# Kernel optimization log

Hardware: AMD Instinct MI355X
Metric: run time of the kernel (lower is better)

The kernel has to match this reference:

```python
import jax, jax.numpy as jnp
import numpy as np

N_NODES = 100000
N_EDGES = 1600000
D_IN = 128
D_OUT = 128
N_GRAPHS = 256


def setup_inputs() -> dict:
    key = jax.random.key(0)
    k1, k2, k3, k4 = jax.random.split(key, 4)
    H = jax.random.normal(k1, (N_NODES, D_IN), dtype=jnp.float32)
    edge_index = jax.random.randint(k2, (2, N_EDGES), 0, N_NODES, dtype=jnp.int64)
    batch = jnp.sort(jax.random.randint(k3, (N_NODES,), 0, N_GRAPHS, dtype=jnp.int64))
    # Kaiming-normal init: std = sqrt(2 / fan_in)
    W = jax.random.normal(k4, (D_IN, D_OUT), dtype=jnp.float32) * np.float32(np.sqrt(2.0 / D_IN))
    return {"H": H, "edge_index": edge_index, "batch": batch, "W": W}


def reference(H, edge_index, batch, W):
    N = H.shape[0]
    src, dst = edge_index[0], edge_index[1]
    # message passing: gather source features, scatter_add into destinations
    agg = jax.ops.segment_sum(H[src], dst, num_segments=N)  # [N, D]
    out = H + agg
    # virtual node: per-graph mean, broadcast back to nodes
    sums = jax.ops.segment_sum(out, batch, num_segments=N_GRAPHS)            # [G, D]
    counts = jax.ops.segment_sum(jnp.ones((N, 1), out.dtype), batch,
                                 num_segments=N_GRAPHS)                       # [G, 1]
    vmean = sums / jnp.maximum(counts, 1.0)
    out = out + vmean[batch]
    # dense transform + activation
    return jax.nn.relu(out @ W)
```

## Files before the change

### kernel.cpp

```cpp
#include <hip/hip_runtime.h>

#define DIM 128
#define NGRAPH 256

#define CHUNK 512
#define CHB 9
#define MAXNB 256
#define EPB 4096
#define EPT (EPB / 256)
#define FCAP 14336

typedef __attribute__((ext_vector_type(8))) short short8;
typedef __attribute__((ext_vector_type(4))) float f32x4;

__device__ inline unsigned int bpack2(float lo, float hi) {
  unsigned int ul = __float_as_uint(lo);
  unsigned int uh = __float_as_uint(hi);
  ul = (ul + 0x7fffu + ((ul >> 16) & 1u)) >> 16;
  uh = (uh + 0x7fffu + ((uh >> 16) & 1u)) & 0xffff0000u;
  return ul | uh;
}

__device__ inline float4 bunpack4(uint2 v) {
  float4 r;
  r.x = __uint_as_float(v.x << 16);
  r.y = __uint_as_float(v.x & 0xffff0000u);
  r.z = __uint_as_float(v.y << 16);
  r.w = __uint_as_float(v.y & 0xffff0000u);
  return r;
}

__global__ __launch_bounds__(256) void k_prep(const float4* __restrict__ H4,
    uint2* __restrict__ Hb, int n4,
    const int* __restrict__ dst, unsigned short* __restrict__ bh, int E,
    int NBLK) {
  __shared__ unsigned int hist[MAXNB];
  int blk = blockIdx.x, t = threadIdx.x;
  int i = blk * 256 + t;
  if (i < n4) {
    float4 a = H4[i];
    uint2 r;
    r.x = bpack2(a.x, a.y);
    r.y = bpack2(a.z, a.w);
    Hb[i] = r;
  }
  if (blk < NBLK) {
    hist[t] = 0;
    __syncthreads();
    int base = blk * EPB;
#pragma unroll
    for (int k = 0; k < EPT; ++k) {
      int e = base + k * 256 + t;
      if (e < E) atomicAdd(&hist[((unsigned)dst[e]) >> CHB], 1);
    }
    __syncthreads();
    bh[(size_t)blk * MAXNB + t] = (unsigned short)hist[t];
  }
}

__global__ __launch_bounds__(256) void k_bhist(const int* __restrict__ dst,
    unsigned short* __restrict__ bh, int E) {
  __shared__ unsigned int hist[MAXNB];
  int blk = blockIdx.x, t = threadIdx.x;
  hist[t] = 0;
  __syncthreads();
  int base = blk * EPB;
#pragma unroll
  for (int i = 0; i < EPT; ++i) {
    int e = base + i * 256 + t;
    if (e < E) atomicAdd(&hist[((unsigned)dst[e]) >> CHB], 1);
  }
  __syncthreads();
  bh[(size_t)blk * MAXNB + t] = (unsigned short)hist[t];
}

__global__ __launch_bounds__(256) void k_bscan(unsigned short* __restrict__ bh,
    unsigned int* __restrict__ btot, int NBLK) {
  __shared__ unsigned int tmp[256];
  int b = blockIdx.x, t = threadIdx.x;
  int i0 = 2 * t, i1 = 2 * t + 1;
  unsigned int a0 = (i0 < NBLK) ? bh[(size_t)i0 * MAXNB + b] : 0u;
  unsigned int a1 = (i1 < NBLK) ? bh[(size_t)i1 * MAXNB + b] : 0u;
  unsigned int ps = a0 + a1;
  tmp[t] = ps;
  __syncthreads();
  for (int off = 1; off < 256; off <<= 1) {
    unsigned int x = (t >= off) ? tmp[t - off] : 0u;
    __syncthreads();
    tmp[t] += x;
    __syncthreads();
  }
  unsigned int ex = tmp[t] - ps;
  if (i0 < NBLK) bh[(size_t)i0 * MAXNB + b] = (unsigned short)ex;
  if (i1 < NBLK) bh[(size_t)i1 * MAXNB + b] = (unsigned short)(ex + a0);
  if (t == 255) btot[b] = tmp[255];
}

__global__ __launch_bounds__(256) void k_bscan2(const unsigned int* __restrict__ btot,
    unsigned int* __restrict__ bbase, int* __restrict__ offs, int N, int E) {
  __shared__ unsigned int s[256];
  int t = threadIdx.x;
  unsigned int v = btot[t];
  s[t] = v;
  __syncthreads();
  for (int off = 1; off < 256; off <<= 1) {
    unsigned int x = (t >= off) ? s[t - off] : 0u;
    __syncthreads();
    s[t] += x;
    __syncthreads();
  }
  bbase[t] = s[t] - v;
  if (t == 255) { bbase[256] = s[255]; offs[N] = E; }
}

__global__ __launch_bounds__(256) void k_part(const int* __restrict__ src,
    const int* __restrict__ dst, const unsigned short* __restrict__ bh,
    const unsigned int* __restrict__ bbase, unsigned int* __restrict__ pack, int E) {
  __shared__ unsigned int hist[MAXNB];
  __shared__ unsigned int sc[MAXNB];
  __shared__ unsigned int gbase[MAXNB];
  __shared__ unsigned int lpack[EPB];
  __shared__ unsigned short lbkt[EPB];
  __shared__ unsigned int totS;
  int blk = blockIdx.x, t = threadIdx.x;
  hist[t] = 0;
  __syncthreads();

  int base = blk * EPB;
  unsigned int pk[EPT];
  int bk[EPT];
  unsigned int rk[EPT];
#pragma unroll
  for (int i = 0; i < EPT; ++i) {
    int e = base + i * 256 + t;
    if (e < E) {
      unsigned int s = (unsigned)src[e], d = (unsigned)dst[e];
      pk[i] = (s << CHB) | (d & (CHUNK - 1));
      int b = (int)(d >> CHB);
      bk[i] = b;
      rk[i] = atomicAdd(&hist[b], 1u);
    } else {
      bk[i] = -1;
    }
  }
  __syncthreads();

  unsigned int c = hist[t];
  sc[t] = c;
  __syncthreads();
  for (int off = 1; off < 256; off <<= 1) {
    unsigned int x = (t >= off) ? sc[t - off] : 0u;
    __syncthreads();
    sc[t] += x;
    __syncthreads();
  }
  if (t == 255) totS = sc[255];
  hist[t] = sc[t] - c;
  gbase[t] = bbase[t] + (unsigned int)bh[(size_t)blk * MAXNB + t];
  __syncthreads();

#pragma unroll
  for (int i = 0; i < EPT; ++i) {
    if (bk[i] >= 0) {
      unsigned int slot = hist[bk[i]] + rk[i];
      lpack[slot] = pk[i];
      lbkt[slot] = (unsigned short)bk[i];
    }
  }
  __syncthreads();

  unsigned int tot = totS;
  for (unsigned int s = t; s < tot; s += 256) {
    int b = lbkt[s];
    unsigned int local = s - hist[b];
    pack[gbase[b] + local] = lpack[s];
  }
}

__global__ __launch_bounds__(256) void k_fine(unsigned int* __restrict__ pack,
    const unsigned int* __restrict__ bbase, int* __restrict__ offs, int N) {
  __shared__ unsigned int lp[FCAP];
  __shared__ unsigned int cnt[CHUNK];
  __shared__ unsigned int cur[CHUNK];
  __shared__ unsigned int tmp[256];
  int b = blockIdx.x, t = threadIdx.x;
  unsigned int lo = bbase[b], hi = bbase[b + 1];
  int n = (int)(hi - lo);
  if (n > FCAP) n = FCAP;
  cnt[2 * t] = 0; cnt[2 * t + 1] = 0;
  __syncthreads();
  for (int i = t; i < n; i += 256) {
    unsigned int p = pack[lo + i];
    lp[i] = p;
    atomicAdd(&cnt[p & (CHUNK - 1)], 1u);
  }
  __syncthreads();
  unsigned int c0 = cnt[2 * t], c1 = cnt[2 * t + 1];
  unsigned int ps = c0 + c1;
  tmp[t] = ps;
  __syncthreads();
  for (int off = 1; off < 256; off <<= 1) {
    unsigned int x = (t >= off) ? tmp[t - off] : 0u;
    __syncthreads();
    tmp[t] += x;
    __syncthreads();
  }
  unsigned int ex = tmp[t] - ps;
  cur[2 * t] = ex;
  cur[2 * t + 1] = ex + c0;
  __syncthreads();
  int nb0 = b * CHUNK;
#pragma unroll
  for (int j = t; j < CHUNK; j += 256) {
    int node = nb0 + j;
    if (node < N) offs[node] = (int)(lo + cur[j]);
  }
  __syncthreads();
  for (int i = t; i < n; i += 256) {
    unsigned int p = lp[i];
    unsigned int r = atomicAdd(&cur[p & (CHUNK - 1)], 1u);
    pack[lo + r] = p;
  }
}

__device__ inline void bacc(uint2 v, float4& a) {
  a.x += __uint_as_float(v.x << 16);
  a.y += __uint_as_float(v.x & 0xffff0000u);
  a.z += __uint_as_float(v.y << 16);
  a.w += __uint_as_float(v.y & 0xffff0000u);
}

__global__ __launch_bounds__(256) void k_gatherbx(const uint2* __restrict__ Hb,
    const int* __restrict__ offs, const unsigned int* __restrict__ pack,
    uint2* __restrict__ Hx, int n) {
  int gid = blockIdx.x * 256 + threadIdx.x;
  int node = gid >> 6;
  if (node >= n) return;
  int lane = threadIdx.x & 63;
  int half = lane >> 5, q = lane & 31;
  float4 A = {0,0,0,0}, B = {0,0,0,0}, C = {0,0,0,0}, D = {0,0,0,0};
  int beg = offs[node], end = offs[node + 1];
  int j = beg + half;
  for (; j + 6 < end; j += 8) {
    uint2 v0 = Hb[(size_t)(pack[j + 0] >> CHB) * 32 + q];
    uint2 v1 = Hb[(size_t)(pack[j + 2] >> CHB) * 32 + q];
    uint2 v2 = Hb[(size_t)(pack[j + 4] >> CHB) * 32 + q];
    uint2 v3 = Hb[(size_t)(pack[j + 6] >> CHB) * 32 + q];
    bacc(v0, A); bacc(v1, B); bacc(v2, C); bacc(v3, D);
  }
  for (; j < end; j += 2) bacc(Hb[(size_t)(pack[j] >> CHB) * 32 + q], A);
  A.x += B.x + (C.x + D.x);
  A.y += B.y + (C.y + D.y);
  A.z += B.z + (C.z + D.z);
  A.w += B.w + (C.w + D.w);
  A.x += __shfl_xor(A.x, 32);
  A.y += __shfl_xor(A.y, 32);
  A.z += __shfl_xor(A.z, 32);
  A.w += __shfl_xor(A.w, 32);
  if (half == 0) {
    float4 b4 = bunpack4(Hb[(size_t)node * 32 + q]);
    uint2 o;
    o.x = bpack2(b4.x + A.x, b4.y + A.y);
    o.y = bpack2(b4.z + A.z, b4.w + A.w);
    Hx[(size_t)node * 32 + q] = o;
  }
}

__global__ __launch_bounds__(256) void k_gatherb(const float* __restrict__ H,
    const uint2* __restrict__ Hb, const int* __restrict__ offs,
    const unsigned int* __restrict__ pack, float* __restrict__ out, int n) {
  int gid = blockIdx.x * 256 + threadIdx.x;
  int node = gid >> 6;
  if (node >= n) return;
  int lane = threadIdx.x & 63;
  int half = lane >> 5, q = lane & 31;
  float4 A = {0,0,0,0}, B = {0,0,0,0}, C = {0,0,0,0}, D = {0,0,0,0};
  int beg = offs[node], end = offs[node + 1];
  int j = beg + half;
  for (; j + 6 < end; j += 8) {
    uint2 v0 = Hb[(size_t)(pack[j + 0] >> CHB) * 32 + q];
    uint2 v1 = Hb[(size_t)(pack[j + 2] >> CHB) * 32 + q];
    uint2 v2 = Hb[(size_t)(pack[j + 4] >> CHB) * 32 + q];
    uint2 v3 = Hb[(size_t)(pack[j + 6] >> CHB) * 32 + q];
    bacc(v0, A); bacc(v1, B); bacc(v2, C); bacc(v3, D);
  }
  for (; j < end; j += 2) bacc(Hb[(size_t)(pack[j] >> CHB) * 32 + q], A);
  A.x += B.x + (C.x + D.x);
  A.y += B.y + (C.y + D.y);
  A.z += B.z + (C.z + D.z);
  A.w += B.w + (C.w + D.w);
  A.x += __shfl_xor(A.x, 32);
  A.y += __shfl_xor(A.y, 32);
  A.z += __shfl_xor(A.z, 32);
  A.w += __shfl_xor(A.w, 32);
  if (half == 0) {
    float4 b4 = ((const float4*)H)[(size_t)node * 32 + q];
    float4 r;
    r.x = b4.x + A.x; r.y = b4.y + A.y; r.z = b4.z + A.z; r.w = b4.w + A.w;
    ((float4*)out)[(size_t)node * 32 + q] = r;
  }
}

__global__ __launch_bounds__(256) void k_gather(const float* __restrict__ H,
    const int* __restrict__ offs, const unsigned int* __restrict__ pack,
    float* __restrict__ out, int n) {
  int gid = blockIdx.x * 256 + threadIdx.x;
  int node = gid >> 6;
  if (node >= n) return;
  int lane = threadIdx.x & 63;
  const float2* H2 = (const float2*)H;
  float2 base = H2[(size_t)node * 64 + lane];
  float2 s0 = {0.f, 0.f}, s1 = {0.f, 0.f};
  int beg = offs[node], end = offs[node + 1];
  int j = beg;
  for (; j + 2 <= end; j += 2) {
    float2 v0 = H2[(size_t)(pack[j + 0] >> CHB) * 64 + lane];
    float2 v1 = H2[(size_t)(pack[j + 1] >> CHB) * 64 + lane];
    s0.x += v0.x; s0.y += v0.y;
    s1.x += v1.x; s1.y += v1.y;
  }
  for (; j < end; ++j) {
    float2 v = H2[(size_t)(pack[j] >> CHB) * 64 + lane];
    s0.x += v.x; s0.y += v.y;
  }
  float2 r;
  r.x = base.x + s0.x + s1.x;
  r.y = base.y + s0.y + s1.y;
  ((float2*)out)[(size_t)node * 64 + lane] = r;
}

__global__ __launch_bounds__(256) void k_init(const float4* __restrict__ s,
                                              float4* __restrict__ d, int n4) {
  int i = blockIdx.x * 256 + threadIdx.x;
  if (i < n4) d[i] = s[i];
}

__global__ __launch_bounds__(256) void k_scatter(const float* __restrict__ H,
    const int* __restrict__ src, const int* __restrict__ dst,
    float* __restrict__ out, int nE) {
  long long idx = (long long)blockIdx.x * 256 + threadIdx.x;
  int e = (int)(idx >> 5);
  if (e >= nE) return;
  int q = (int)(idx & 31);
  int s = src[e];
  int t = dst[e];
  const float4 h = *(const float4*)(H + (size_t)s * DIM + q * 4);
  float* o = out + (size_t)t * DIM + q * 4;
  unsafeAtomicAdd(o + 0, h.x);
  unsafeAtomicAdd(o + 1, h.y);
  unsafeAtomicAdd(o + 2, h.z);
  unsafeAtomicAdd(o + 3, h.w);
}

__global__ __launch_bounds__(256) void k_vmean4x(const uint2* __restrict__ hx,
    const int* __restrict__ batch, float* __restrict__ vmean, int n) {
  int g = blockIdx.x >> 2, c = blockIdx.x & 3;
  int lo = 0, hi = n;
  while (lo < hi) { int m = (lo + hi) >> 1; if (batch[m] < g) lo = m + 1; else hi = m; }
  int start = lo;
  hi = n;
  while (lo < hi) { int m = (lo + hi) >> 1; if (batch[m] < g + 1) lo = m + 1; else hi = m; }
  int end = lo;

  int t = threadIdx.x, rg = t >> 3, s = t & 7;
  int d4 = c * 8 + s;
  float4 acc = {0,0,0,0};
  for (int r = start + rg; r < end; r += 32) {
    float4 v = bunpack4(hx[(size_t)r * 32 + d4]);
    acc.x += v.x; acc.y += v.y; acc.z += v.z; acc.w += v.w;
  }
  __shared__ float4 sd[256];
  sd[t] = acc;
  __syncthreads();
  for (int off = 16; off >= 1; off >>= 1) {
    if (rg < off) {
      float4 o = sd[t + off * 8];
      acc.x += o.x; acc.y += o.y; acc.z += o.z; acc.w += o.w;
      sd[t] = acc;
    }
    __syncthreads();
  }
  if (rg == 0) {
    float cnt = fmaxf((float)(end - start), 1.0f);
    float4 r;
    r.x = acc.x / cnt; r.y = acc.y / cnt; r.z = acc.z / cnt; r.w = acc.w / cnt;
    ((float4*)vmean)[g * 32 + d4] = r;
  }
}

__global__ __launch_bounds__(256) void k_vmean4(const float* __restrict__ x,
    const int* __restrict__ batch, float* __restrict__ vmean, int n) {
  int g = blockIdx.x >> 2, c = blockIdx.x & 3;
  int lo = 0, hi = n;
  while (lo < hi) { int m = (lo + hi) >> 1; if (batch[m] < g) lo = m + 1; else hi = m; }
  int start = lo;
  hi = n;
  while (lo < hi) { int m = (lo + hi) >> 1; if (batch[m] < g + 1) lo = m + 1; else hi = m; }
  int end = lo;

  int t = threadIdx.x, rg = t >> 3, s = t & 7;
  int d4 = c * 8 + s;
  const float4* x4 = (const float4*)x;
  float4 acc = {0,0,0,0};
  for (int r = start + rg; r < end; r += 32) {
    float4 v = x4[(size_t)r * 32 + d4];
    acc.x += v.x; acc.y += v.y; acc.z += v.z; acc.w += v.w;
  }
  __shared__ float4 sd[256];
  sd[t] = acc;
  __syncthreads();
  for (int off = 16; off >= 1; off >>= 1) {
    if (rg < off) {
      float4 o = sd[t + off * 8];
      acc.x += o.x; acc.y += o.y; acc.z += o.z; acc.w += o.w;
      sd[t] = acc;
    }
    __syncthreads();
  }
  if (rg == 0) {
    float cnt = fmaxf((float)(end - start), 1.0f);
    float4 r;
    r.x = acc.x / cnt; r.y = acc.y / cnt; r.z = acc.z / cnt; r.w = acc.w / cnt;
    ((float4*)vmean)[g * 32 + d4] = r;
  }
}

__global__ __launch_bounds__(256) void k_wprep(const float* __restrict__ W,
                                               uint4* __restrict__ wt) {
  int gid = blockIdx.x * 256 + threadIdx.x;
  int col = gid >> 4, chunk = gid & 15;
  float f[8];
#pragma unroll
  for (int j = 0; j < 8; ++j) f[j] = W[(chunk * 8 + j) * DIM + col];
  uint4 u;
  u.x = bpack2(f[0], f[1]);
  u.y = bpack2(f[2], f[3]);
  u.z = bpack2(f[4], f[5]);
  u.w = bpack2(f[6], f[7]);
  wt[col * 16 + (chunk ^ (col & 7))] = u;
}

__global__ __launch_bounds__(256) void k_mfmax(const uint4* __restrict__ Hx,
    float* __restrict__ io, const int* __restrict__ batch,
    const float* __restrict__ vmean, const uint4* __restrict__ wt, int n) {
  __shared__ uint4 WtL[2048];
  int tid = threadIdx.x;
#pragma unroll
  for (int j = 0; j < 8; ++j) WtL[tid + 256 * j] = wt[tid + 256 * j];
  __syncthreads();

  int wid = tid >> 6;
  int lane = tid & 63;
  int q = lane & 15, hi = lane >> 4;
  int row0 = blockIdx.x * 128 + wid * 32;

  f32x4 acc[2][8];
#pragma unroll
  for (int m = 0; m < 2; ++m)
#pragma unroll
    for (int nn = 0; nn < 8; ++nn) acc[m][nn] = (f32x4){0.f, 0.f, 0.f, 0.f};

  bool okm[2];
  const uint4* xrow[2];
  const float4* vrow[2];
#pragma unroll
  for (int m = 0; m < 2; ++m) {
    int row = row0 + m * 16 + q;
    bool ok = row < n;
    okm[m] = ok;
    int g = ok ? batch[row] : 0;
    xrow[m] = Hx + (size_t)row * 16;
    vrow[m] = (const float4*)vmean + (size_t)g * 32;
  }

  for (int kk = 0; kk < 4; ++kk) {
    short8 Bf[8];
#pragma unroll
    for (int nn = 0; nn < 8; ++nn) {
      int colrow = nn * 16 + q;
      int idx = colrow * 16 + ((kk * 4 + hi) ^ (colrow & 7));
      Bf[nn] = *(short8*)&WtL[idx];
    }
    short8 Af[2];
#pragma unroll
    for (int m = 0; m < 2; ++m) {
      uint4 u = {0, 0, 0, 0};
      if (okm[m]) {
        uint4 xv = xrow[m][kk * 4 + hi];
        float4 x0 = bunpack4(*(uint2*)&xv.x);
        float4 x1 = bunpack4(*(uint2*)&xv.z);
        int c = kk * 8 + hi * 2;
        float4 v0 = vrow[m][c], v1 = vrow[m][c + 1];
        u.x = bpack2(x0.x + v0.x, x0.y + v0.y);
        u.y = bpack2(x0.z + v0.z, x0.w + v0.w);
        u.z = bpack2(x1.x + v1.x, x1.y + v1.y);
        u.w = bpack2(x1.z + v1.z, x1.w + v1.w);
      }
      Af[m] = *(short8*)&u;
    }
#pragma unroll
    for (int nn = 0; nn < 8; ++nn) {
      acc[0][nn] = __builtin_amdgcn_mfma_f32_16x16x32_bf16(Af[0], Bf[nn], acc[0][nn], 0, 0, 0);
      acc[1][nn] = __builtin_amdgcn_mfma_f32_16x16x32_bf16(Af[1], Bf[nn], acc[1][nn], 0, 0, 0);
    }
  }

#pragma unroll
  for (int m = 0; m < 2; ++m) {
    int grow0 = row0 + m * 16 + hi * 4;
#pragma unroll
    for (int nn = 0; nn < 8; ++nn) {
      int gcol = nn * 16 + q;
      f32x4 c = acc[m][nn];
#pragma unroll
      for (int r = 0; r < 4; ++r) {
        int grow = grow0 + r;
        if (grow < n) io[(size_t)grow * DIM + gcol] = fmaxf(c[r], 0.f);
      }
    }
  }
}

__global__ __launch_bounds__(256) void k_mfma(float* __restrict__ io,
    const int* __restrict__ batch, const float* __restrict__ vmean,
    const uint4* __restrict__ wt, int n) {
  __shared__ uint4 WtL[2048];
  int tid = threadIdx.x;
#pragma unroll
  for (int j = 0; j < 8; ++j) WtL[tid + 256 * j] = wt[tid + 256 * j];
  __syncthreads();

  int wid = tid >> 6;
  int lane = tid & 63;
  int q = lane & 15, hi = lane >> 4;
  int row0 = blockIdx.x * 128 + wid * 32;

  f32x4 acc[2][8];
#pragma unroll
  for (int m = 0; m < 2; ++m)
#pragma unroll
    for (int nn = 0; nn < 8; ++nn) acc[m][nn] = (f32x4){0.f, 0.f, 0.f, 0.f};

  bool okm[2];
  const float4* xrow[2];
  const float4* vrow[2];
#pragma unroll
  for (int m = 0; m < 2; ++m) {
    int row = row0 + m * 16 + q;
    bool ok = row < n;
    okm[m] = ok;
    int g = ok ? batch[row] : 0;
    xrow[m] = (const float4*)io + (size_t)row * 32;
    vrow[m] = (const float4*)vmean + (size_t)g * 32;
  }

  for (int kk = 0; kk < 4; ++kk) {
    short8 Bf[8];
#pragma unroll
    for (int nn = 0; nn < 8; ++nn) {
      int colrow = nn * 16 + q;
      int idx = colrow * 16 + ((kk * 4 + hi) ^ (colrow & 7));
      Bf[nn] = *(short8*)&WtL[idx];
    }
    short8 Af[2];
#pragma unroll
    for (int m = 0; m < 2; ++m) {
      float4 x0 = {0,0,0,0}, x1 = {0,0,0,0};
      if (okm[m]) {
        int c = kk * 8 + hi * 2;
        float4 a0 = xrow[m][c], a1 = xrow[m][c + 1];
        float4 v0 = vrow[m][c], v1 = vrow[m][c + 1];
        x0.x = a0.x + v0.x; x0.y = a0.y + v0.y; x0.z = a0.z + v0.z; x0.w = a0.w + v0.w;
        x1.x = a1.x + v1.x; x1.y = a1.y + v1.y; x1.z = a1.z + v1.z; x1.w = a1.w + v1.w;
      }
      uint4 u;
      u.x = bpack2(x0.x, x0.y);
      u.y = bpack2(x0.z, x0.w);
      u.z = bpack2(x1.x, x1.y);
      u.w = bpack2(x1.z, x1.w);
      Af[m] = *(short8*)&u;
    }
#pragma unroll
    for (int nn = 0; nn < 8; ++nn) {
      acc[0][nn] = __builtin_amdgcn_mfma_f32_16x16x32_bf16(Af[0], Bf[nn], acc[0][nn], 0, 0, 0);
      acc[1][nn] = __builtin_amdgcn_mfma_f32_16x16x32_bf16(Af[1], Bf[nn], acc[1][nn], 0, 0, 0);
    }
  }

#pragma unroll
  for (int m = 0; m < 2; ++m) {
    int grow0 = row0 + m * 16 + hi * 4;
#pragma unroll
    for (int nn = 0; nn < 8; ++nn) {
      int gcol = nn * 16 + q;
      f32x4 c = acc[m][nn];
#pragma unroll
      for (int r = 0; r < 4; ++r) {
        int grow = grow0 + r;
        if (grow < n) io[(size_t)grow * DIM + gcol] = fmaxf(c[r], 0.f);
      }
    }
  }
}

#define TRR 64
__global__ __launch_bounds__(256) void k_gemm(float* __restrict__ io,
    const int* __restrict__ batch, const float* __restrict__ vmean,
    const float* __restrict__ W, int n) {
  __shared__ float xs[TRR][DIM + 1];
  __shared__ float Wl[DIM][64];
  int tid = threadIdx.x;
  int row0 = blockIdx.x * TRR;

  for (int i = tid; i < TRR * 32; i += 256) {
    int r = i >> 5, c4 = i & 31;
    int row = row0 + r;
    float4 a;
    if (row < n) {
      int g = batch[row];
      float4 xv = *((const float4*)(io + (size_t)row * DIM) + c4);
      float4 vv = *((const float4*)(vmean + (size_t)g * DIM) + c4);
      a.x = xv.x + vv.x; a.y = xv.y + vv.y; a.z = xv.z + vv.z; a.w = xv.w + vv.w;
    } else {
      a.x = a.y = a.z = a.w = 0.f;
    }
    xs[r][c4 * 4 + 0] = a.x;
    xs[r][c4 * 4 + 1] = a.y;
    xs[r][c4 * 4 + 2] = a.z;
    xs[r][c4 * 4 + 3] = a.w;
  }

  int cg = tid & 15;
  int rg = tid >> 4;
  float acc[4][4];

  for (int jh = 0; jh < 2; ++jh) {
    __syncthreads();
    for (int i = tid; i < DIM * 16; i += 256) {
      int k = i >> 4, c4 = i & 15;
      *(float4*)&Wl[k][c4 * 4] =
          *(const float4*)(W + (size_t)k * DIM + jh * 64 + c4 * 4);
    }
    __syncthreads();

#pragma unroll
    for (int a = 0; a < 4; ++a)
#pragma unroll
      for (int b = 0; b < 4; ++b) acc[a][b] = 0.f;

    for (int k = 0; k < DIM; ++k) {
      float4 wv = *(const float4*)&Wl[k][cg * 4];
#pragma unroll
      for (int a = 0; a < 4; ++a) {
        float xv = xs[rg * 4 + a][k];
        acc[a][0] += xv * wv.x;
        acc[a][1] += xv * wv.y;
        acc[a][2] += xv * wv.z;
        acc[a][3] += xv * wv.w;
      }
    }

#pragma unroll
    for (int a = 0; a < 4; ++a) {
      int row = row0 + rg * 4 + a;
      if (row < n) {
        float4 o;
        o.x = fmaxf(acc[a][0], 0.f);
        o.y = fmaxf(acc[a][1], 0.f);
        o.z = fmaxf(acc[a][2], 0.f);
        o.w = fmaxf(acc[a][3], 0.f);
        *(float4*)(io + (size_t)row * DIM + jh * 64 + cg * 4) = o;
      }
    }
  }
}

extern "C" void kernel_launch(void* const* d_in, const int* in_sizes, int n_in,
                              void* d_out, int out_size, void* d_ws, size_t ws_size,
                              hipStream_t stream) {
  const float* H     = (const float*)d_in[0];
  const int*   ei    = (const int*)d_in[1];
  const int*   batch = (const int*)d_in[2];
  const float* W     = (const float*)d_in[3];
  float* out = (float*)d_out;

  int N = in_sizes[0] / DIM;
  int E = in_sizes[1] / 2;
  const int* src = ei;
  const int* dst = ei + E;

  int NB   = (N + CHUNK - 1) >> CHB;
  int NBLK = (E + EPB - 1) / EPB;

  size_t o = 0;
  auto carve = [&](size_t bytes) -> void* {
    void* p = (char*)d_ws + o;
    o = (o + bytes + 255) & ~(size_t)255;
    return p;
  };
  unsigned int*   pack  = (unsigned int*)carve((size_t)E * 4);
  int*            offs  = (int*)carve(((size_t)N + 1) * 4);
  unsigned short* bh    = (unsigned short*)carve((size_t)NBLK * MAXNB * 2);
  unsigned int*   btot  = (unsigned int*)carve(MAXNB * 4);
  unsigned int*   bbase = (unsigned int*)carve((MAXNB + 1) * 4);
  size_t o_csr = o;
  uint2*          Hb    = (uint2*)carve((size_t)N * DIM * 2);
  size_t o_bf = o;
  uint4*          wt    = (uint4*)carve((size_t)DIM * DIM * 2);
  size_t o_wt = o;
  uint2*          Hx    = (uint2*)carve((size_t)N * DIM * 2);
  size_t o_hx = o;
  float* vmean = (float*)bh;

  bool csr_ok = (o_csr <= ws_size) && (NB >= 1) && (NB <= MAXNB) &&
                (NBLK <= 512) && ((size_t)NBLK * MAXNB * 2 >= (size_t)NGRAPH * DIM * 4) &&
                (E / NB <= 8192);
  bool bf_ok = csr_ok && (o_bf <= ws_size);
  bool wt_ok = bf_ok && (o_wt <= ws_size) && (DIM == 128);
  bool hx_ok = wt_ok && (o_hx <= ws_size);

  if (csr_ok) {
    if (bf_ok) {
      int n4 = N * DIM / 4;
      int gprep = (n4 + 255) / 256;
      if (gprep < NBLK) gprep = NBLK;
      k_prep<<<gprep, 256, 0, stream>>>((const float4*)H, Hb, n4, dst, bh, E, NBLK);
    } else {
      k_bhist<<<NBLK, 256, 0, stream>>>(dst, bh, E);
    }
    k_bscan<<<MAXNB, 256, 0, stream>>>(bh, btot, NBLK);
    k_bscan2<<<1, 256, 0, stream>>>(btot, bbase, offs, N, E);
    k_part<<<NBLK, 256, 0, stream>>>(src, dst, bh, bbase, pack, E);
    k_fine<<<NB, 256, 0, stream>>>(pack, bbase, offs, N);
    long long gthreads = (long long)N * 64;
    int gblocks = (int)((gthreads + 255) / 256);
    if (hx_ok) {
      k_gatherbx<<<gblocks, 256, 0, stream>>>(Hb, offs, pack, Hx, N);
      k_vmean4x<<<NGRAPH * 4, 256, 0, stream>>>(Hx, batch, vmean, N);
      k_wprep<<<8, 256, 0, stream>>>(W, wt);
      k_mfmax<<<(N + 127) / 128, 256, 0, stream>>>((const uint4*)Hx, out, batch, vmean, wt, N);
      return;
    }
    if (bf_ok) {
      k_gatherb<<<gblocks, 256, 0, stream>>>(H, Hb, offs, pack, out, N);
    } else {
      k_gather<<<gblocks, 256, 0, stream>>>(H, offs, pack, out, N);
    }
  } else {
    vmean = (float*)d_ws;
    int n4 = N * DIM / 4;
    k_init<<<(n4 + 255) / 256, 256, 0, stream>>>((const float4*)H, (float4*)out, n4);
    long long sthreads = (long long)E * 32;
    k_scatter<<<(int)((sthreads + 255) / 256), 256, 0, stream>>>(H, src, dst, out, E);
  }

  k_vmean4<<<NGRAPH * 4, 256, 0, stream>>>(out, batch, vmean, N);

  if (wt_ok) {
    k_wprep<<<8, 256, 0, stream>>>(W, wt);
    k_mfma<<<(N + 127) / 128, 256, 0, stream>>>(out, batch, vmean, wt, N);
  } else {
    k_gemm<<<(N + TRR - 1) / TRR, 256, 0, stream>>>(out, batch, vmean, W, N);
  }
}
```

Before: 159.2 us.

## Fold W prep into k_prep, split vmean add into separate pass, nontemporal IO

Weight transpose/packing moves into the k_prep kernel, which saves one launch. The virtual-node mean add moves out of the MFMA kernel into a new elementwise k_vadd pass over the bf16 Hx buffer, so the GEMM loads its A fragments directly. Nontemporal hints are added to the H load and the output store. The extra pass reads and writes Hx one more time (about 25 MB each way) and costs a launch, which may outweigh the simpler GEMM inner loop.

```diff
diff --git a/kernel.cpp b/kernel.cpp
--- a/kernel.cpp
+++ b/kernel.cpp
@@ -30,19 +30,32 @@
   return r;
 }
 
-__global__ __launch_bounds__(256) void k_prep(const float4* __restrict__ H4,
+__global__ __launch_bounds__(256) void k_prep(const float* __restrict__ Hf,
     uint2* __restrict__ Hb, int n4,
     const int* __restrict__ dst, unsigned short* __restrict__ bh, int E,
-    int NBLK) {
+    int NBLK, const float* __restrict__ W, uint4* __restrict__ wt, int dowt) {
   __shared__ unsigned int hist[MAXNB];
   int blk = blockIdx.x, t = threadIdx.x;
   int i = blk * 256 + t;
   if (i < n4) {
-    float4 a = H4[i];
+    f32x4 a = __builtin_nontemporal_load((const f32x4*)Hf + i);
     uint2 r;
     r.x = bpack2(a.x, a.y);
     r.y = bpack2(a.z, a.w);
     Hb[i] = r;
+  }
+  if (dowt && blk < 8) {
+    int gid = blk * 256 + t;
+    int col = gid >> 4, chunk = gid & 15;
+    float f[8];
+#pragma unroll
+    for (int j = 0; j < 8; ++j) f[j] = W[(chunk * 8 + j) * DIM + col];
+    uint4 u;
+    u.x = bpack2(f[0], f[1]);
+    u.y = bpack2(f[2], f[3]);
+    u.z = bpack2(f[4], f[5]);
+    u.w = bpack2(f[6], f[7]);
+    wt[col * 16 + (chunk ^ (col & 7))] = u;
   }
   if (blk < NBLK) {
     hist[t] = 0;
@@ -425,6 +438,20 @@
   }
 }
 
+__global__ __launch_bounds__(256) void k_vadd(uint2* __restrict__ Hx,
+    const int* __restrict__ batch, const float* __restrict__ vmean, int n32) {
+  int i = blockIdx.x * 256 + threadIdx.x;
+  if (i >= n32) return;
+  int node = i >> 5, c4 = i & 31;
+  int g = batch[node];
+  float4 x = bunpack4(Hx[i]);
+  float4 v = ((const float4*)vmean)[(size_t)g * 32 + c4];
+  uint2 o;
+  o.x = bpack2(x.x + v.x, x.y + v.y);
+  o.y = bpack2(x.z + v.z, x.w + v.w);
+  Hx[i] = o;
+}
+
 __global__ __launch_bounds__(256) void k_wprep(const float* __restrict__ W,
                                                uint4* __restrict__ wt) {
   int gid = blockIdx.x * 256 + threadIdx.x;
@@ -440,9 +467,8 @@
   wt[col * 16 + (chunk ^ (col & 7))] = u;
 }
 
-__global__ __launch_bounds__(256) void k_mfmax(const uint4* __restrict__ Hx,
-    float* __restrict__ io, const int* __restrict__ batch,
-    const float* __restrict__ vmean, const uint4* __restrict__ wt, int n) {
+__global__ __launch_bounds__(256) void k_mfmax2(const uint4* __restrict__ Hx,
+    float* __restrict__ io, const uint4* __restrict__ wt, int n) {
   __shared__ uint4 WtL[2048];
   int tid = threadIdx.x;
 #pragma unroll
@@ -462,15 +488,11 @@
 
   bool okm[2];
   const uint4* xrow[2];
-  const float4* vrow[2];
 #pragma unroll
   for (int m = 0; m < 2; ++m) {
     int row = row0 + m * 16 + q;
-    bool ok = row < n;
-    okm[m] = ok;
-    int g = ok ? batch[row] : 0;
+    okm[m] = row < n;
     xrow[m] = Hx + (size_t)row * 16;
-    vrow[m] = (const float4*)vmean + (size_t)g * 32;
   }
 
   for (int kk = 0; kk < 4; ++kk) {
@@ -485,17 +507,7 @@
 #pragma unroll
     for (int m = 0; m < 2; ++m) {
       uint4 u = {0, 0, 0, 0};
-      if (okm[m]) {
-        uint4 xv = xrow[m][kk * 4 + hi];
-        float4 x0 = bunpack4(*(uint2*)&xv.x);
-        float4 x1 = bunpack4(*(uint2*)&xv.z);
-        int c = kk * 8 + hi * 2;
-        float4 v0 = vrow[m][c], v1 = vrow[m][c + 1];
-        u.x = bpack2(x0.x + v0.x, x0.y + v0.y);
-        u.y = bpack2(x0.z + v0.z, x0.w + v0.w);
-        u.z = bpack2(x1.x + v1.x, x1.y + v1.y);
-        u.w = bpack2(x1.z + v1.z, x1.w + v1.w);
-      }
+      if (okm[m]) u = xrow[m][kk * 4 + hi];
       Af[m] = *(short8*)&u;
     }
 #pragma unroll
@@ -515,7 +527,8 @@
 #pragma unroll
       for (int r = 0; r < 4; ++r) {
         int grow = grow0 + r;
-        if (grow < n) io[(size_t)grow * DIM + gcol] = fmaxf(c[r], 0.f);
+        if (grow < n)
+          __builtin_nontemporal_store(fmaxf(c[r], 0.f), &io[(size_t)grow * DIM + gcol]);
       }
     }
   }
@@ -724,7 +737,8 @@
       int n4 = N * DIM / 4;
       int gprep = (n4 + 255) / 256;
       if (gprep < NBLK) gprep = NBLK;
-      k_prep<<<gprep, 256, 0, stream>>>((const float4*)H, Hb, n4, dst, bh, E, NBLK);
+      k_prep<<<gprep, 256, 0, stream>>>(H, Hb, n4, dst, bh, E, NBLK,
+                                        W, wt, hx_ok ? 1 : 0);
     } else {
       k_bhist<<<NBLK, 256, 0, stream>>>(dst, bh, E);
     }
@@ -737,8 +751,9 @@
     if (hx_ok) {
       k_gatherbx<<<gblocks, 256, 0, stream>>>(Hb, offs, pack, Hx, N);
       k_vmean4x<<<NGRAPH * 4, 256, 0, stream>>>(Hx, batch, vmean, N);
-      k_wprep<<<8, 256, 0, stream>>>(W, wt);
-      k_mfmax<<<(N + 127) / 128, 256, 0, stream>>>((const uint4*)Hx, out, batch, vmean, wt, N);
+      int n32 = N * 32;
+      k_vadd<<<(n32 + 255) / 256, 256, 0, stream>>>(Hx, batch, vmean, n32);
+      k_mfmax2<<<(N + 127) / 128, 256, 0, stream>>>((const uint4*)Hx, out, wt, N);
       return;
     }
     if (bf_ok) {
```

Result: slower. 170.6 us (+7.2%).
